# Performance work log

Hardware: AMD Instinct MI355X
Metric: run time of the kernel (lower is better)

The kernel has to match this reference:

```python
import jax, jax.numpy as jnp
from jax import lax
import numpy as np

B, P, C = 16, 21824, 2          # batch, num_priors, num_classes
KCAND = 1024                    # candidate cap for jittable NMS
TOP_K = 750
CONF_THRESH = 0.3
IOU_THRESH = 0.01
VAR = (0.1, 0.2)
IMG_SCALE = 1024.0


def setup_inputs() -> dict:
    key = jax.random.key(0)
    k1, k2, k3 = jax.random.split(key, 3)
    return {
        "boxes_logits": jax.random.normal(k1, (B, P, 4), dtype=jnp.float32),
        "cls_logits": jax.random.normal(k2, (B, P, C), dtype=jnp.float32),
        "priors": jax.random.uniform(k3, (P, 4), dtype=jnp.float32),
    }


def decode(loc, priors):
    # priors are (cx, cy, w, h); loc are SSD-style offsets
    xy = priors[..., :2] + loc[..., :2] * VAR[0] * priors[..., 2:]
    wh = priors[..., 2:] * jnp.exp(loc[..., 2:] * VAR[1])
    x1y1 = xy - wh * 0.5
    x2y2 = x1y1 + wh
    return jnp.concatenate([x1y1, x2y2], axis=-1) * IMG_SCALE


def iou_matrix(b):
    # b: [K,4] in x1y1x2y2; torchvision-style IoU (areas unclamped, inter clamped)
    area = (b[:, 2] - b[:, 0]) * (b[:, 3] - b[:, 1])
    lt = jnp.maximum(b[:, None, :2], b[None, :, :2])
    rb = jnp.minimum(b[:, None, 2:], b[None, :, 2:])
    wh = jnp.clip(rb - lt, 0.0)
    inter = wh[..., 0] * wh[..., 1]
    union = area[:, None] + area[None, :] - inter
    return inter / jnp.maximum(union, 1e-9)


def greedy_nms(iou, valid, thresh):
    # boxes assumed sorted by descending score; returns keep mask [K]
    K = iou.shape[0]
    iou = jnp.where(jnp.eye(K, dtype=bool), 0.0, iou)  # ignore self-overlap

    def step(suppressed, i):
        keep_i = jnp.logical_and(~suppressed[i], valid[i])
        suppressed = jnp.logical_or(suppressed, keep_i & (iou[i] > thresh))
        return suppressed, keep_i

    _, keep = lax.scan(step, jnp.zeros(K, dtype=bool), jnp.arange(K))
    return keep


def _detect_one(boxes, scores_all):
    # boxes [P,4], scores_all [P,C]
    scores = scores_all[:, 1:].reshape(-1)                        # drop background
    labels = jnp.broadcast_to(jnp.arange(1, C), (P, C - 1)).reshape(-1)
    bx = jnp.broadcast_to(boxes[:, None, :], (P, C - 1, 4)).reshape(-1, 4)

    masked = jnp.where(scores > CONF_THRESH, scores, -1.0)
    top_scores, idx = lax.top_k(masked, KCAND)                    # score-sorted candidates
    cb = bx[idx]                                                  # [K,4]
    cl = labels[idx]                                              # [K]
    valid = top_scores > CONF_THRESH

    # batched_nms: offset boxes per class so classes never overlap
    max_c = jnp.max(jnp.where(valid[:, None], cb, 0.0))
    off = cl.astype(cb.dtype)[:, None] * (max_c + 1.0)
    keep = greedy_nms(iou_matrix(cb + off), valid, IOU_THRESH)

    kept_scores = jnp.where(keep, top_scores, -1.0)
    final_s, kidx = lax.top_k(kept_scores, TOP_K)                 # keep[:top_k] in score order
    mask = keep[kidx]
    out_boxes = jnp.where(mask[:, None], cb[kidx], 0.0)
    out_scores = jnp.where(mask, final_s, 0.0)
    out_labels = jnp.where(mask, cl[kidx], 0)
    return out_boxes, out_scores, out_labels, mask


def reference(boxes_logits, cls_logits, priors):
    scores_logits = jax.nn.softmax(cls_logits, axis=2)            # [B,P,C]
    boxes = decode(boxes_logits, priors)                          # [B,P,4]
    pred_boxes, pred_scores, pred_labels, mask = jax.vmap(_detect_one)(boxes, scores_logits)
    return pred_boxes, pred_scores, pred_labels, mask
```

## Files before the change

### kernel.cpp

```cpp
#include <hip/hip_runtime.h>

typedef unsigned long long u64;
typedef unsigned int u32;

#define KC 1024
#define TOPK 750
#define CONF 0.3f
#define IOU_T 0.01f
#define WINB 0x2F80u
#define NW 128
#define CCAP 2048

__device__ __forceinline__ u64 score_key(const float* __restrict__ c2, u32 p) {
    float a0 = c2[0], a1 = c2[1];
    float m  = fmaxf(a0, a1);
    float e0 = expf(a0 - m), e1 = expf(a1 - m);
    float s  = e1 / (e0 + e1);
    float ms = s > CONF ? s : -1.0f;
    u32 u = __float_as_uint(ms);
    u32 mapped = (u & 0x80000000u) ? ~u : (u | 0x80000000u);
    return ((u64)mapped << 32) | (u32)(~p);
}

__global__ __launch_bounds__(1024) void k_sel(const float* __restrict__ cls,
        const float* __restrict__ bl, const float* __restrict__ priors,
        u64* __restrict__ csorted, float* __restrict__ cboxes,
        float* __restrict__ coffs, int P) {
    int b = blockIdx.x, tid = threadIdx.x;
    __shared__ u32 sh[NW], sa[NW], sb_[NW], sufx[NW], bfill[NW];
    __shared__ int sh_cut;
    __shared__ u32 sh_T;
    __shared__ u64 keys2[CCAP];
    __shared__ u64 ksorted[KC];
    __shared__ float smax[KC];

    if (tid < NW) { sh[tid] = 0; bfill[tid] = 0; }
    if (tid == 0) sh_cut = 0;
    ksorted[tid] = 0;
    __syncthreads();

    const float* cb2 = cls + (size_t)b * P * 2;
    for (int i = tid; i < P; i += 1024) {
        u64 k = score_key(cb2 + (size_t)i * 2, (u32)i);
        u32 wbin = (u32)(k >> 50) - WINB;
        if (wbin < (u32)NW) atomicAdd(&sh[wbin], 1u);
    }
    __syncthreads();
    if (tid < NW) sa[tid] = sh[tid];
    __syncthreads();
    u32 *src = sa, *dst = sb_;
    for (int d = 1; d < NW; d <<= 1) {
        if (tid < NW) dst[tid] = src[tid] + ((tid + d < NW) ? src[tid + d] : 0u);
        __syncthreads();
        u32* tmp = src; src = dst; dst = tmp;
    }
    if (tid < NW && src[tid] >= KC) atomicMax(&sh_cut, tid);
    __syncthreads();
    int cutw = sh_cut;
    if (tid < NW) sufx[tid] = src[tid] - sh[tid];
    if (tid == 0) sh_T = src[cutw];
    __syncthreads();

    for (int i = tid; i < P; i += 1024) {
        u64 k = score_key(cb2 + (size_t)i * 2, (u32)i);
        u32 wbin = (u32)(k >> 50) - WINB;
        if (wbin < (u32)NW && (int)wbin >= cutw) {
            u32 pos = sufx[wbin] + atomicAdd(&bfill[wbin], 1u);
            if (pos < CCAP) keys2[pos] = k;
        }
    }
    __syncthreads();

    u32 T = sh_T; if (T > CCAP) T = CCAP;
    for (int c = tid; c < (int)T; c += 1024) {
        u64 key = keys2[c];
        u32 w = (u32)(key >> 50) - WINB;
        u32 seg0 = sufx[w];
        u32 segN = seg0 + sh[w];
        if (segN > T) segN = T;
        u32 cnt = 0;
        for (u32 j = seg0; j < segN; ++j) cnt += (keys2[j] > key) ? 1u : 0u;
        u32 r = seg0 + cnt;
        if (r < KC) ksorted[r] = key;
    }
    __syncthreads();

    u64 key = ksorted[tid];
    bool valid = (key != 0ull);
    float4 bx; bx.x = bx.y = bx.z = bx.w = 0.0f;
    if (valid) {
        u32 p = ~(u32)(key & 0xffffffffull);
        const float* pr4 = priors + (size_t)p * 4;
        const float* lc  = bl + ((size_t)b * P + p) * 4;
        float pcx = pr4[0], pcy = pr4[1], pw = pr4[2], ph = pr4[3];
        float lx = lc[0], ly = lc[1], lw = lc[2], lh = lc[3];
        float cx = pcx + lx * 0.1f * pw;
        float cy = pcy + ly * 0.1f * ph;
        float ww = pw * expf(lw * 0.2f);
        float hh = ph * expf(lh * 0.2f);
        float t1x = cx - ww * 0.5f;
        float t1y = cy - hh * 0.5f;
        bx.x = t1x * 1024.0f;
        bx.y = t1y * 1024.0f;
        bx.z = (t1x + ww) * 1024.0f;
        bx.w = (t1y + hh) * 1024.0f;
    }
    csorted[(size_t)b * KC + tid] = key;
    reinterpret_cast<float4*>(cboxes)[(size_t)b * KC + tid] = bx;
    smax[tid] = valid ? fmaxf(fmaxf(bx.x, bx.y), fmaxf(bx.z, bx.w)) : 0.0f;
    __syncthreads();
    for (int st = 512; st > 0; st >>= 1) {
        if (tid < st) smax[tid] = fmaxf(smax[tid], smax[tid + st]);
        __syncthreads();
    }
    if (tid == 0) coffs[b] = smax[0] + 1.0f;
}

__global__ __launch_bounds__(1024) void k_iou(const float* __restrict__ cboxes,
        const float* __restrict__ coffs, u64* __restrict__ rows) {
    int b = blockIdx.y, tid = threadIdx.x;
    __shared__ float sx1[KC], sy1[KC], sx2[KC], sy2[KC], sar[KC];
    float off = coffs[b];
    float4 bx = reinterpret_cast<const float4*>(cboxes)[(size_t)b * KC + tid];
    float xs1 = bx.x + off, ys1 = bx.y + off, xs2 = bx.z + off, ys2 = bx.w + off;
    sx1[tid] = xs1; sy1[tid] = ys1; sx2[tid] = xs2; sy2[tid] = ys2;
    sar[tid] = (xs2 - xs1) * (ys2 - ys1);
    __syncthreads();

    int w = tid >> 6, lane = tid & 63;
    u64* rbb = rows + (size_t)b * KC * 16;
    #pragma unroll
    for (int rr = 0; rr < 4; ++rr) {
        int r = blockIdx.x * 64 + w * 4 + rr;
        float rx1 = sx1[r], ry1 = sy1[r], rx2 = sx2[r], ry2 = sy2[r], rar = sar[r];
        u64* rb = rbb + (size_t)r * 16;
        #pragma unroll 4
        for (int c = 0; c < 16; ++c) {
            int col = c * 64 + lane;
            float ltx = fmaxf(rx1, sx1[col]), lty = fmaxf(ry1, sy1[col]);
            float rbx = fminf(rx2, sx2[col]), rby = fminf(ry2, sy2[col]);
            float w2 = fmaxf(rbx - ltx, 0.0f), h2 = fmaxf(rby - lty, 0.0f);
            float inter = w2 * h2;
            float uni = rar + sar[col] - inter;
            float iou = inter / fmaxf(uni, 1e-9f);
            bool pred = (iou > IOU_T) && (col != r);
            u64 m = __ballot(pred);
            if (lane == 0) rb[c] = m;
        }
    }
}

__global__ __launch_bounds__(1024) void k_scan(const u64* __restrict__ csorted,
        const u64* __restrict__ rows, const float* __restrict__ cboxes,
        float* __restrict__ out, int B) {
    int b = blockIdx.x, tid = threadIdx.x;
    __shared__ u64 vw[16], keepw[16];
    u64 key = csorted[(size_t)b * KC + tid];
    bool valid = (key != 0ull);
    u32 mapped = (u32)(key >> 32);
    u32 fb = (mapped & 0x80000000u) ? (mapped & 0x7fffffffu) : ~mapped;
    float score = __uint_as_float(fb);
    u64 bal = __ballot(valid);
    if ((tid & 63) == 0) vw[tid >> 6] = bal;
    __syncthreads();

    if (tid < 16) {
        int lane = tid;
        u64 supp = ~vw[lane];
        u64 kw = 0;
        const u64* rb = rows + (size_t)b * KC * 16;
        for (int w = 0; w < 16; ++w) {
            u64 sw = __shfl(supp, w);
            u64 rem = ~sw;
            while (rem) {
                int bit = __ffsll((long long)rem) - 1;
                int i = w * 64 + bit;
                supp |= rb[(size_t)i * 16 + lane];
                if (lane == w) kw |= 1ull << bit;
                sw = __shfl(supp, w);
                u64 above = (bit == 63) ? 0ull : (~0ull << (bit + 1));
                rem = ~sw & above;
            }
        }
        keepw[lane] = kw;
    }
    __syncthreads();

    int wq = tid >> 6, bq = tid & 63;
    u64 myw = keepw[wq];
    bool kept = (myw >> bq) & 1ull;
    int rank = 0, nk = 0;
    #pragma unroll
    for (int w2 = 0; w2 < 16; ++w2) {
        int pc = __popcll(keepw[w2]);
        nk += pc;
        if (w2 < wq) rank += pc;
    }
    rank += __popcll(myw & ((1ull << bq) - 1ull));

    float* ob  = out;
    float* osc = out + (size_t)B * TOPK * 4;
    float* olb = osc + (size_t)B * TOPK;
    float* omk = olb + (size_t)B * TOPK;

    if (kept && rank < TOPK) {
        size_t o = (size_t)b * TOPK + rank;
        float4 bx = reinterpret_cast<const float4*>(cboxes)[(size_t)b * KC + tid];
        *reinterpret_cast<float4*>(ob + o * 4) = bx;
        osc[o] = score;
        olb[o] = 1.0f;
        omk[o] = 1.0f;
    }
    int zstart = nk < TOPK ? nk : TOPK;
    if (tid >= zstart && tid < TOPK) {
        size_t o = (size_t)b * TOPK + tid;
        float4 z; z.x = z.y = z.z = z.w = 0.0f;
        *reinterpret_cast<float4*>(ob + o * 4) = z;
        osc[o] = 0.0f;
        olb[o] = 0.0f;
        omk[o] = 0.0f;
    }
}

extern "C" void kernel_launch(void* const* d_in, const int* in_sizes, int n_in,
                              void* d_out, int out_size, void* d_ws, size_t ws_size,
                              hipStream_t stream) {
    const float* boxes_logits = (const float*)d_in[0];
    const float* cls_logits   = (const float*)d_in[1];
    const float* priors       = (const float*)d_in[2];
    int P = in_sizes[2] / 4;
    int B = in_sizes[0] / (P * 4);
    float* out = (float*)d_out;
    char* wsb = (char*)d_ws;

    size_t CSORT_B = (size_t)B * KC * sizeof(u64);
    size_t CBOX_B  = (size_t)B * KC * 4 * sizeof(float);
    size_t COFF_B  = 256;
    u64*   csorted = (u64*)wsb;
    float* cboxes  = (float*)(wsb + CSORT_B);
    float* coffs   = (float*)(wsb + CSORT_B + CBOX_B);
    u64*   rows    = (u64*)(wsb + CSORT_B + CBOX_B + COFF_B);

    hipLaunchKernelGGL(k_sel,  dim3(B),         dim3(1024), 0, stream,
                       cls_logits, boxes_logits, priors, csorted, cboxes, coffs, P);
    hipLaunchKernelGGL(k_iou,  dim3(KC / 64, B), dim3(1024), 0, stream,
                       cboxes, coffs, rows);
    hipLaunchKernelGGL(k_scan, dim3(B),         dim3(1024), 0, stream,
                       csorted, rows, cboxes, out, B);
}
```

Measured before the change: 145.9 us.

## Split score-key computation and histogram into a grid-wide pre-pass kernel

Adds a k_gather kernel launched over many blocks per batch that computes softmax score keys once, writes them to workspace, and emits per-block bin histograms. The selection kernel, which runs one block per batch, now reduces those partial histograms and reads precomputed keys instead of computing softmax twice over P priors. The aim is to spread the P-wide pass across the whole GPU instead of only 16 blocks. The cost is an extra kernel launch and a global write/read of the keys array.

```diff
diff --git a/kernel.cpp b/kernel.cpp
--- a/kernel.cpp
+++ b/kernel.cpp
@@ -22,31 +22,53 @@
     return ((u64)mapped << 32) | (u32)(~p);
 }
 
-__global__ __launch_bounds__(1024) void k_sel(const float* __restrict__ cls,
+__global__ __launch_bounds__(256) void k_gather(const float* __restrict__ cls,
+        u64* __restrict__ keys, u32* __restrict__ histseg, int P, int NBLK) {
+    __shared__ u32 lh[NW];
+    int t = threadIdx.x, blk = blockIdx.x, b = blockIdx.y;
+    if (t < NW) lh[t] = 0;
+    __syncthreads();
+    int p = blk * 256 + t;
+    if (p < P) {
+        u64 k = score_key(cls + ((size_t)b * P + p) * 2, (u32)p);
+        keys[(size_t)b * P + p] = k;
+        u32 wbin = (u32)(k >> 50) - WINB;
+        if (wbin < (u32)NW) atomicAdd(&lh[wbin], 1u);
+    }
+    __syncthreads();
+    if (t < NW) histseg[((size_t)b * NBLK + blk) * NW + t] = lh[t];
+}
+
+__global__ __launch_bounds__(1024) void k_sel2(const u64* __restrict__ keys,
         const float* __restrict__ bl, const float* __restrict__ priors,
-        u64* __restrict__ csorted, float* __restrict__ cboxes,
-        float* __restrict__ coffs, int P) {
+        const u32* __restrict__ histseg, u64* __restrict__ csorted,
+        float* __restrict__ cboxes, float* __restrict__ coffs, int P, int NBLK) {
     int b = blockIdx.x, tid = threadIdx.x;
     __shared__ u32 sh[NW], sa[NW], sb_[NW], sufx[NW], bfill[NW];
+    __shared__ u32 partial[8 * NW];
     __shared__ int sh_cut;
     __shared__ u32 sh_T;
     __shared__ u64 keys2[CCAP];
     __shared__ u64 ksorted[KC];
     __shared__ float smax[KC];
 
-    if (tid < NW) { sh[tid] = 0; bfill[tid] = 0; }
+    {
+        int bin = tid & 127, c = tid >> 7;
+        u32 s = 0;
+        for (int j = c; j < NBLK; j += 8)
+            s += histseg[((size_t)b * NBLK + j) * NW + bin];
+        partial[c * NW + bin] = s;
+    }
+    if (tid < NW) bfill[tid] = 0;
     if (tid == 0) sh_cut = 0;
     ksorted[tid] = 0;
     __syncthreads();
-
-    const float* cb2 = cls + (size_t)b * P * 2;
-    for (int i = tid; i < P; i += 1024) {
-        u64 k = score_key(cb2 + (size_t)i * 2, (u32)i);
-        u32 wbin = (u32)(k >> 50) - WINB;
-        if (wbin < (u32)NW) atomicAdd(&sh[wbin], 1u);
-    }
-    __syncthreads();
-    if (tid < NW) sa[tid] = sh[tid];
+    if (tid < NW) {
+        u32 tot = 0;
+        #pragma unroll
+        for (int c = 0; c < 8; ++c) tot += partial[c * NW + tid];
+        sh[tid] = tot; sa[tid] = tot;
+    }
     __syncthreads();
     u32 *src = sa, *dst = sb_;
     for (int d = 1; d < NW; d <<= 1) {
@@ -61,8 +83,9 @@
     if (tid == 0) sh_T = src[cutw];
     __syncthreads();
 
+    const u64* kb = keys + (size_t)b * P;
     for (int i = tid; i < P; i += 1024) {
-        u64 k = score_key(cb2 + (size_t)i * 2, (u32)i);
+        u64 k = kb[i];
         u32 wbin = (u32)(k >> 50) - WINB;
         if (wbin < (u32)NW && (int)wbin >= cutw) {
             u32 pos = sufx[wbin] + atomicAdd(&bfill[wbin], 1u);
@@ -230,21 +253,28 @@
     const float* priors       = (const float*)d_in[2];
     int P = in_sizes[2] / 4;
     int B = in_sizes[0] / (P * 4);
+    int NBLK = (P + 255) / 256;
     float* out = (float*)d_out;
     char* wsb = (char*)d_ws;
 
+    size_t KEYS_B  = (size_t)B * P * sizeof(u64);
+    size_t HSEG_B  = (size_t)B * NBLK * NW * sizeof(u32);
     size_t CSORT_B = (size_t)B * KC * sizeof(u64);
     size_t CBOX_B  = (size_t)B * KC * 4 * sizeof(float);
     size_t COFF_B  = 256;
-    u64*   csorted = (u64*)wsb;
-    float* cboxes  = (float*)(wsb + CSORT_B);
-    float* coffs   = (float*)(wsb + CSORT_B + CBOX_B);
-    u64*   rows    = (u64*)(wsb + CSORT_B + CBOX_B + COFF_B);
-
-    hipLaunchKernelGGL(k_sel,  dim3(B),         dim3(1024), 0, stream,
-                       cls_logits, boxes_logits, priors, csorted, cboxes, coffs, P);
-    hipLaunchKernelGGL(k_iou,  dim3(KC / 64, B), dim3(1024), 0, stream,
+    u64*   keys    = (u64*)wsb;
+    u32*   histseg = (u32*)(wsb + KEYS_B);
+    u64*   csorted = (u64*)(wsb + KEYS_B + HSEG_B);
+    float* cboxes  = (float*)(wsb + KEYS_B + HSEG_B + CSORT_B);
+    float* coffs   = (float*)(wsb + KEYS_B + HSEG_B + CSORT_B + CBOX_B);
+    u64*   rows    = (u64*)(wsb + KEYS_B + HSEG_B + CSORT_B + CBOX_B + COFF_B);
+
+    hipLaunchKernelGGL(k_gather, dim3(NBLK, B),    dim3(256),  0, stream,
+                       cls_logits, keys, histseg, P, NBLK);
+    hipLaunchKernelGGL(k_sel2,   dim3(B),          dim3(1024), 0, stream,
+                       keys, boxes_logits, priors, histseg, csorted, cboxes, coffs, P, NBLK);
+    hipLaunchKernelGGL(k_iou,    dim3(KC / 64, B), dim3(1024), 0, stream,
                        cboxes, coffs, rows);
-    hipLaunchKernelGGL(k_scan, dim3(B),         dim3(1024), 0, stream,
+    hipLaunchKernelGGL(k_scan,   dim3(B),          dim3(1024), 0, stream,
                        csorted, rows, cboxes, out, B);
 }
```

Result: faster. 138.4 us (-5.2%).
